# Optimization experiments

Measured on AMD Instinct MI355X. Metric: run time of the kernel, lower is better.

## Reference

```python
import jax, jax.numpy as jnp
import numpy as np
from jax import lax

B, T, V, E, H, DA, R, S, A, NR = 256, 64, 30000, 300, 512, 350, 16, 64, 16, 3


def setup_inputs() -> dict:
    key = jax.random.key(0)
    ks = jax.random.split(key, 24)

    def gn(k, shape, scale):
        return (jax.random.normal(k, shape) * scale).astype(jnp.float32)

    def xavier(k, shape):
        fan = sum(shape[-2:]) if len(shape) >= 2 else shape[0] * 2
        return (jax.random.uniform(k, shape, minval=-1.0, maxval=1.0)
                * np.sqrt(6.0 / fan)).astype(jnp.float32)

    s = 1.0 / np.sqrt(H)
    inp = {
        "tokens": jax.random.randint(ks[0], (B, T), 0, V),
        "lengths": jnp.full((B,), T, dtype=jnp.int32),
        "embedding": gn(ks[1], (V, E), 0.02),
        # BiLSTM layer 0 (input E), layer 1 (input 2H); gates order i,f,g,o (PyTorch)
        "Wih_l0f": gn(ks[2], (4 * H, E), s), "Whh_l0f": gn(ks[3], (4 * H, H), s), "b_l0f": jnp.zeros((4 * H,), jnp.float32),
        "Wih_l0b": gn(ks[4], (4 * H, E), s), "Whh_l0b": gn(ks[5], (4 * H, H), s), "b_l0b": jnp.zeros((4 * H,), jnp.float32),
        "Wih_l1f": gn(ks[6], (4 * H, 2 * H), s), "Whh_l1f": gn(ks[7], (4 * H, H), s), "b_l1f": jnp.zeros((4 * H,), jnp.float32),
        "Wih_l1b": gn(ks[8], (4 * H, 2 * H), s), "Whh_l1b": gn(ks[9], (4 * H, H), s), "b_l1b": jnp.zeros((4 * H,), jnp.float32),
        "ws1": xavier(ks[10], (DA, 2 * H)),
        "ws2": xavier(ks[11], (R, DA)),
        "caps_W": xavier(ks[12], (R, 2 * H, S * A)),
    }
    return inp


def _lstm_dir(x, Wih, Whh, b, reverse=False):
    # x: [T, B, D] -> hidden states [T, B, H]
    if reverse:
        x = x[::-1]
    h0 = jnp.zeros((x.shape[1], Whh.shape[1]), x.dtype)
    c0 = jnp.zeros_like(h0)

    def step(carry, xt):
        h, c = carry
        z = xt @ Wih.T + h @ Whh.T + b
        i, f, g, o = jnp.split(z, 4, axis=-1)
        c = jax.nn.sigmoid(f) * c + jax.nn.sigmoid(i) * jnp.tanh(g)
        h = jax.nn.sigmoid(o) * jnp.tanh(c)
        return (h, c), h

    _, hs = lax.scan(step, (h0, c0), x)
    return hs[::-1] if reverse else hs


def reference(tokens, lengths, embedding,
              Wih_l0f, Whh_l0f, b_l0f, Wih_l0b, Whh_l0b, b_l0b,
              Wih_l1f, Whh_l1f, b_l1f, Wih_l1b, Whh_l1b, b_l1b,
              ws1, ws2, caps_W):
    # Embedding + 2-layer BiLSTM (all lengths == T, so packing is a no-op).
    x = embedding[tokens].transpose(1, 0, 2)          # [T, B, E]
    l0 = jnp.concatenate([_lstm_dir(x, Wih_l0f, Whh_l0f, b_l0f),
                          _lstm_dir(x, Wih_l0b, Whh_l0b, b_l0b, True)], -1)
    l1 = jnp.concatenate([_lstm_dir(l0, Wih_l1f, Whh_l1f, b_l1f),
                          _lstm_dir(l0, Wih_l1b, Whh_l1b, b_l1b, True)], -1)
    outp = l1.transpose(1, 0, 2)                      # [B, T, 2H]

    # Self-attention pooling (note: original applies NO softmax on alphas).
    hbar = jnp.tanh(jnp.einsum('bte,ae->bta', outp, ws1))   # [B, T, DA]
    alphas = jnp.einsum('bta,ra->btr', hbar, ws2)           # [B, T, R]
    attention = alphas.transpose(0, 2, 1)                   # [B, R, T]
    sent = jnp.einsum('brt,bte->bre', attention, outp)      # [B, R, 2H]

    # Capsule votes + dynamic routing.
    votes = jnp.einsum('bri,rio->bro', sent, caps_W).reshape(B, R, S, A)
    logits = jnp.zeros((B, R, S), votes.dtype)
    for _ in range(NR):
        route = jax.nn.softmax(logits, axis=2)
        preact = jnp.einsum('brs,brsa->bsa', route, votes)  # [B, S, A]
        norm = jnp.linalg.norm(preact, axis=2, keepdims=True)
        act = preact / norm * (norm * norm / (0.5 + norm * norm))
        logits = logits + jnp.einsum('brsa,bsa->brs', votes, act)
    class_logits = jnp.linalg.norm(act, axis=-1)            # [B, S]
    return (sent, class_logits)
```

## Files before the change

kernel.cpp:

```cpp
#include <hip/hip_runtime.h>
#include <stdint.h>

#define PB 256
#define PT 64
#define PE 300
#define PH 512
#define PDA 350
#define PR 16
#define PS 64
#define PA 16

typedef __attribute__((ext_vector_type(8))) short short8;
typedef __attribute__((ext_vector_type(4))) float f4;
typedef unsigned long long u64;

__device__ __forceinline__ float bf2f(unsigned short u) {
    unsigned v = ((unsigned)u) << 16;
    return __builtin_bit_cast(float, v);
}
__device__ __forceinline__ unsigned short f2bf(float f) {
    unsigned u = __builtin_bit_cast(unsigned int, f);
    u = u + 0x7fffu + ((u >> 16) & 1u);
    return (unsigned short)(u >> 16);
}
__device__ __forceinline__ float sigf(float x) { return 1.f / (1.f + __expf(-x)); }
__device__ __forceinline__ float tanhf_(float x) { return 1.f - 2.f / (1.f + __expf(2.f * x)); }


__global__ __launch_bounds__(256) void k_embed(const int* __restrict__ tokens,
                                               const float* __restrict__ emb,
                                               unsigned short* __restrict__ X) {
    int idx = blockIdx.x * 256 + threadIdx.x;
    if (idx >= 16384 * 320) return;
    int row = idx / 320, e = idx - row * 320;
    int t = row >> 8, b = row & 255;
    float v = 0.f;
    if (e < 300) v = emb[(long)tokens[b * 64 + t] * 300 + e];
    X[idx] = f2bf(v);
}

__global__ __launch_bounds__(256) void k_cvt_pad(const float* __restrict__ src,
                                                 unsigned short* __restrict__ dst,
                                                 int N, int K, int N2, int K2) {
    int idx = blockIdx.x * 256 + threadIdx.x;
    if (idx >= N2 * K2) return;
    int n = idx / K2, k = idx - n * K2;
    float v = (n < N && k < K) ? src[(long)n * K + k] : 0.f;
    dst[idx] = f2bf(v);
}

__global__ __launch_bounds__(256) void k_capsT(const float* __restrict__ src,
                                               unsigned short* __restrict__ dst) {
    __shared__ float tile[32][33];
    int r = blockIdx.x, kb = blockIdx.y * 32, nb = blockIdx.z * 32;
    int tx = threadIdx.x & 31, ty = threadIdx.x >> 5;
    for (int i = 0; i < 32; i += 8)
        tile[ty + i][tx] = src[((long)r << 20) + (long)(kb + ty + i) * 1024 + nb + tx];
    __syncthreads();
    for (int i = 0; i < 32; i += 8)
        dst[((long)r << 20) + (long)(nb + ty + i) * 1024 + kb + tx] = f2bf(tile[tx][ty + i]);
}

__global__ __launch_bounds__(256) void k_whh_shuf(const float* __restrict__ W,
                                                  unsigned short* __restrict__ dst) {
    int idx = blockIdx.x * 256 + threadIdx.x;
    int el = idx & 7, lane = (idx >> 3) & 63, ks = (idx >> 9) & 15, nt = (idx >> 13) & 7, hs = idx >> 16;
    int gcol = (nt >> 1) * 512 + hs * 32 + (nt & 1) * 16 + (lane & 15);
    int k = ks * 32 + (lane >> 4) * 8 + el;
    dst[idx] = f2bf(W[(long)gcol * 512 + k]);
}

template <int OUT_BF16, int TANH>
__global__ __launch_bounds__(256) void k_gemm(const unsigned short* __restrict__ A,
                                              const unsigned short* __restrict__ W,
                                              void* __restrict__ Cv,
                                              const float* __restrict__ bias,
                                              int K, int lda, int ldc,
                                              long aOffZ, long wOffZ, long cOffZ, long bOffZ) {
    A += blockIdx.z * aOffZ;
    W += blockIdx.z * wOffZ;
    if (bias) bias += blockIdx.z * bOffZ;
    const long cbase = blockIdx.z * cOffZ;
    const int m0 = blockIdx.x * 128, n0 = blockIdx.y * 128;
    __shared__ unsigned short As[4096], Bs[4096];
    const int w = threadIdx.x >> 6, l = threadIdx.x & 63;
    const int wm = w & 1, wn = w >> 1;
    const int fr = l & 15, fk = (l >> 4) * 8;
    f4 acc[4][4] = {};
    for (int k0 = 0; k0 < K; k0 += 32) {
        __syncthreads();
#pragma unroll
        for (int i = 0; i < 2; i++) {
            int tI = w + i * 4;
            const unsigned short* ga = A + (long)(m0 + tI * 16 + fr) * lda + k0 + fk;
            const unsigned short* gb = W + (long)(n0 + tI * 16 + fr) * K + k0 + fk;
            *(short8*)&As[tI * 512 + l * 8] = *(const short8*)ga;
            *(short8*)&Bs[tI * 512 + l * 8] = *(const short8*)gb;
        }
        __syncthreads();
        short8 av[4], bv[4];
#pragma unroll
        for (int mt = 0; mt < 4; mt++) av[mt] = *(short8*)&As[(wm * 4 + mt) * 512 + l * 8];
#pragma unroll
        for (int nt = 0; nt < 4; nt++) bv[nt] = *(short8*)&Bs[(wn * 4 + nt) * 512 + l * 8];
#pragma unroll
        for (int mt = 0; mt < 4; mt++)
#pragma unroll
            for (int nt = 0; nt < 4; nt++)
                acc[mt][nt] = __builtin_amdgcn_mfma_f32_16x16x32_bf16(av[mt], bv[nt], acc[mt][nt], 0, 0, 0);
    }
#pragma unroll
    for (int mt = 0; mt < 4; mt++) {
        int row = m0 + wm * 64 + mt * 16 + (l >> 4) * 4;
#pragma unroll
        for (int nt = 0; nt < 4; nt++) {
            int col = n0 + wn * 64 + nt * 16 + (l & 15);
            float bb = bias ? bias[col] : 0.f;
#pragma unroll
            for (int i = 0; i < 4; i++) {
                float v = acc[mt][nt][i] + bb;
                if (TANH) v = tanhf_(v);
                long off = cbase + (long)(row + i) * ldc + col;
                if (OUT_BF16)
                    ((unsigned short*)Cv)[off] = f2bf(v);
                else
                    ((float*)Cv)[off] = v;
            }
        }
    }
}

__global__ __launch_bounds__(256, 1) void k_lstm(const unsigned short* __restrict__ Zx,
                                                 const unsigned short* __restrict__ Wshuf,
                                                 unsigned short* __restrict__ hsteps,
                                                 unsigned short* __restrict__ Lout,
                                                 unsigned* __restrict__ cnt) {
    extern __shared__ char smem[];
    unsigned short* Wl = (unsigned short*)smem;
    const int bid = blockIdx.x;
    const int dir = bid >> 6, bg = (bid >> 4) & 3, hs = bid & 15;
    const int tid = threadIdx.x;
    const int l = tid & 63;
    const int w = tid >> 6;
    const int mt2 = w & 1, hc2 = w >> 1;

    {
        const short8* src = (const short8*)(Wshuf + ((long)(dir * 16 + hs) << 16));
        short8* dst = (short8*)Wl;
        for (int i = tid; i < 8192; i += 256) dst[i] = src[i];
    }
    {
        unsigned short* hz = hsteps + (long)dir * (256 * 512);
        for (int i = tid; i < 1024; i += 256) {
            int r = i >> 4, c2 = i & 15;
            __hip_atomic_store((unsigned*)&hz[(bg * 64 + r) * 512 + hs * 32 + c2 * 2], 0u,
                               __ATOMIC_RELAXED, __HIP_MEMORY_SCOPE_AGENT);
        }
    }
    unsigned* myc = cnt + (dir * 4 + bg) * 32;
    asm volatile("s_waitcnt vmcnt(0)" ::: "memory");
    __syncthreads();
    if (tid == 0) __hip_atomic_fetch_add(myc, 1u, __ATOMIC_RELAXED, __HIP_MEMORY_SCOPE_AGENT);

    float c_reg[8];
#pragma unroll
    for (int i = 0; i < 8; i++) c_reg[i] = 0.f;

    const int jg = hs * 32 + hc2 * 16 + (l & 15);
    int rowg_[2][4];
#pragma unroll
    for (int i2 = 0; i2 < 2; i2++)
#pragma unroll
        for (int i = 0; i < 4; i++)
            rowg_[i2][i] = bg * 64 + (mt2 * 2 + i2) * 16 + (l >> 4) * 4 + i;

    for (int step = 0; step < 64; step++) {
        const int t_eff = dir ? (63 - step) : step;
        const unsigned short* zbase = Zx + ((long)dir * 16384 + (long)t_eff * 256) * 2048;

        unsigned short zpre[2][4][4];
#pragma unroll
        for (int i2 = 0; i2 < 2; i2++)
#pragma unroll
            for (int i = 0; i < 4; i++) {
                const unsigned short* zrow = zbase + (long)rowg_[i2][i] * 2048 + jg;
#pragma unroll
                for (int g = 0; g < 4; g++) zpre[i2][i][g] = zrow[g * 512];
            }

        if (tid == 0) {
            unsigned target = 16u * (unsigned)(step + 1);
            while (__hip_atomic_load(myc, __ATOMIC_RELAXED, __HIP_MEMORY_SCOPE_AGENT) < target) {}
        }
        __syncthreads();

        const unsigned short* hb = hsteps + ((long)step * 2 + dir) * (256 * 512);
        const unsigned short* pa0 = hb + (bg * 64 + (mt2 * 2 + 0) * 16 + (l & 15)) * 512 + (l >> 4) * 8;
        const unsigned short* pa1 = hb + (bg * 64 + (mt2 * 2 + 1) * 16 + (l & 15)) * 512 + (l >> 4) * 8;
        short8 a0[16], a1[16];
#pragma unroll
        for (int ks = 0; ks < 16; ks++) {
            a0[ks] = *(const short8*)(pa0 + ks * 32);
            a1[ks] = *(const short8*)(pa1 + ks * 32);
        }
        asm volatile("" ::: "memory");

        f4 acc[2][4] = {};
#pragma unroll
        for (int ks = 0; ks < 16; ks++) {
#pragma unroll
            for (int s = 0; s < 4; s++) {
                int nt = s * 2 + hc2;
                short8 b = *(short8*)&Wl[((nt * 16 + ks) * 64 + l) * 8];
                acc[0][s] = __builtin_amdgcn_mfma_f32_16x16x32_bf16(a0[ks], b, acc[0][s], 0, 0, 0);
                acc[1][s] = __builtin_amdgcn_mfma_f32_16x16x32_bf16(a1[ks], b, acc[1][s], 0, 0, 0);
            }
        }

        unsigned short hv[2][4];
        unsigned short* hw = hsteps + ((long)(step + 1) * 2 + dir) * (256 * 512);
#pragma unroll
        for (int i2 = 0; i2 < 2; i2++)
#pragma unroll
            for (int i = 0; i < 4; i++) {
                float zi = acc[i2][0][i] + bf2f(zpre[i2][i][0]);
                float zf = acc[i2][1][i] + bf2f(zpre[i2][i][1]);
                float zg = acc[i2][2][i] + bf2f(zpre[i2][i][2]);
                float zo = acc[i2][3][i] + bf2f(zpre[i2][i][3]);
                int ci = i2 * 4 + i;
                float c = sigf(zf) * c_reg[ci] + sigf(zi) * tanhf_(zg);
                c_reg[ci] = c;
                float h = sigf(zo) * tanhf_(c);
                unsigned short hb16 = f2bf(h);
                hv[i2][i] = hb16;
                __hip_atomic_store(&hw[(long)rowg_[i2][i] * 512 + jg], hb16,
                                   __ATOMIC_RELAXED, __HIP_MEMORY_SCOPE_AGENT);
            }
        asm volatile("s_waitcnt vmcnt(0)" ::: "memory");
        __syncthreads();
        if (tid == 0) __hip_atomic_fetch_add(myc, 1u, __ATOMIC_RELAXED, __HIP_MEMORY_SCOPE_AGENT);

#pragma unroll
        for (int i2 = 0; i2 < 2; i2++)
#pragma unroll
            for (int i = 0; i < 4; i++)
                Lout[((long)t_eff * 256 + rowg_[i2][i]) * 1024 + dir * 512 + jg] = hv[i2][i];
    }
}

__global__ __launch_bounds__(256) void k_alphas(const unsigned short* __restrict__ hbar,
                                                const unsigned short* __restrict__ ws2,
                                                float* __restrict__ att) {
    int w = threadIdx.x >> 6, l = threadIdx.x & 63;
    int mtile = blockIdx.x * 4 + w;
    f4 acc = {};
    const unsigned short* arow = hbar + (long)(mtile * 16 + (l & 15)) * 384 + (l >> 4) * 8;
    const unsigned short* brow = ws2 + (long)(l & 15) * 384 + (l >> 4) * 8;
    for (int ks = 0; ks < 12; ks++) {
        short8 a = *(const short8*)&arow[ks * 32];
        short8 b = *(const short8*)&brow[ks * 32];
        acc = __builtin_amdgcn_mfma_f32_16x16x32_bf16(a, b, acc, 0, 0, 0);
    }
    int r = l & 15;
#pragma unroll
    for (int i = 0; i < 4; i++) {
        int bt = mtile * 16 + (l >> 4) * 4 + i;
        int b = bt & 255, t = bt >> 8;
        att[((long)b * 16 + r) * 64 + t] = acc[i];
    }
}

__global__ __launch_bounds__(256) void k_sent(const float* __restrict__ att,
                                              const unsigned short* __restrict__ L1,
                                              float* __restrict__ sent,
                                              unsigned short* __restrict__ sentb) {
    int b = blockIdx.x, n0 = blockIdx.y * 128;
    __shared__ float al[1024];
    for (int i = threadIdx.x; i < 1024; i += 256) al[i] = att[(long)b * 1024 + i];
    __syncthreads();
    int n = n0 + (threadIdx.x & 127);
    int rh = (threadIdx.x >> 7) * 8;
    float acc[8] = {};
    for (int t = 0; t < 64; t++) {
        float x = bf2f(L1[((long)t * 256 + b) * 1024 + n]);
#pragma unroll
        for (int r = 0; r < 8; r++) acc[r] += al[(rh + r) * 64 + t] * x;
    }
#pragma unroll
    for (int r = 0; r < 8; r++) {
        long o = ((long)b * 16 + rh + r) * 1024 + n;
        sent[o] = acc[r];
        sentb[o] = f2bf(acc[r]);
    }
}

__global__ __launch_bounds__(256) void k_route(const float* __restrict__ votes,
                                               float* __restrict__ clog) {
    __shared__ float v[16384];
    __shared__ float logits[1024];
    __shared__ float route[1024];
    __shared__ float pre[1024];
    __shared__ float act[1024];
    __shared__ float cl[64];
    int b = blockIdx.x, tid = threadIdx.x;
    for (int i = tid; i < 4096; i += 256) ((f4*)v)[i] = ((const f4*)(votes + (long)b * 16384))[i];
    for (int i = tid; i < 1024; i += 256) logits[i] = 0.f;
    __syncthreads();
    for (int it = 0; it < 3; it++) {
        if (tid < 16) {
            float m = -1e30f;
            for (int s = 0; s < 64; s++) m = fmaxf(m, logits[tid * 64 + s]);
            float sum = 0.f;
            for (int s = 0; s < 64; s++) {
                float e = __expf(logits[tid * 64 + s] - m);
                route[tid * 64 + s] = e;
                sum += e;
            }
            float inv = 1.f / sum;
            for (int s = 0; s < 64; s++) route[tid * 64 + s] *= inv;
        }
        __syncthreads();
#pragma unroll
        for (int k = 0; k < 4; k++) {
            int p = k * 256 + tid;
            int s = p >> 4, a = p & 15;
            float acc = 0.f;
            for (int r = 0; r < 16; r++) acc += route[r * 64 + s] * v[(r * 64 + s) * 16 + a];
            pre[p] = acc;
        }
        __syncthreads();
        if (tid < 64) {
            float nsq = 0.f;
            for (int a = 0; a < 16; a++) nsq += pre[tid * 16 + a] * pre[tid * 16 + a];
            float norm = sqrtf(nsq);
            float sc = norm / (0.5f + nsq);
            for (int a = 0; a < 16; a++) act[tid * 16 + a] = pre[tid * 16 + a] * sc;
            cl[tid] = nsq / (0.5f + nsq);
        }
        __syncthreads();
#pragma unroll
        for (int k = 0; k < 4; k++) {
            int p = k * 256 + tid;
            int r = p >> 6, s = p & 63;
            float acc = 0.f;
            for (int a = 0; a < 16; a++) acc += v[(r * 64 + s) * 16 + a] * act[s * 16 + a];
            logits[p] += acc;
        }
        __syncthreads();
    }
    if (tid < 64) clog[(long)b * 64 + tid] = cl[tid];
}

extern "C" void kernel_launch(void* const* d_in, const int* in_sizes, int n_in,
                              void* d_out, int out_size, void* d_ws, size_t ws_size,
                              hipStream_t stream) {
    const int* tokens = (const int*)d_in[0];
    const float* embedding = (const float*)d_in[2];
    const float* Wih_l0f = (const float*)d_in[3];
    const float* Whh_l0f = (const float*)d_in[4];
    const float* b_l0f = (const float*)d_in[5];
    const float* Wih_l0b = (const float*)d_in[6];
    const float* Whh_l0b = (const float*)d_in[7];
    const float* b_l0b = (const float*)d_in[8];
    const float* Wih_l1f = (const float*)d_in[9];
    const float* Whh_l1f = (const float*)d_in[10];
    const float* b_l1f = (const float*)d_in[11];
    const float* Wih_l1b = (const float*)d_in[12];
    const float* Whh_l1b = (const float*)d_in[13];
    const float* b_l1b = (const float*)d_in[14];
    const float* ws1 = (const float*)d_in[15];
    const float* ws2 = (const float*)d_in[16];
    const float* caps_W = (const float*)d_in[17];
    float* out = (float*)d_out;

    char* ws = (char*)d_ws;
    size_t o = 0;
    unsigned short* Xb16 = (unsigned short*)(ws + o); o += (size_t)16384 * 320 * 2;
    unsigned short* ZxL = (unsigned short*)(ws + o); size_t zx_off = o; o += (size_t)2 * 16384 * 2048 * 2;
    unsigned short* L0 = (unsigned short*)(ws + o); o += (size_t)16384 * 1024 * 2;
    unsigned short* L1 = (unsigned short*)(ws + o); o += (size_t)16384 * 1024 * 2;
    unsigned short* Wl0b = (unsigned short*)(ws + o); o += (size_t)2 * 2048 * 320 * 2;
    unsigned short* Wl1b = (unsigned short*)(ws + o); o += (size_t)2 * 2048 * 1024 * 2;
    unsigned short* Wsh0 = (unsigned short*)(ws + o); o += (size_t)2 * 1048576 * 2;
    unsigned short* Wsh1 = (unsigned short*)(ws + o); o += (size_t)2 * 1048576 * 2;
    unsigned short* ws1b = (unsigned short*)(ws + o); o += (size_t)384 * 1024 * 2;
    unsigned short* ws2b = (unsigned short*)(ws + o); o += (size_t)16 * 384 * 2 + 192;
    float* biasc = (float*)(ws + o); o += (size_t)4 * 2048 * 4;
    unsigned* cnts = (unsigned*)(ws + o); o += 4096;
    unsigned short* hsteps = (unsigned short*)(ws + o);
    unsigned short* capsT = (unsigned short*)(ws + o);
    o += (size_t)65 * 2 * 256 * 512 * 2;
    unsigned short* hbarb = (unsigned short*)(ws + zx_off);
    float* att = (float*)(ws + zx_off + (size_t)16384 * 384 * 2);
    unsigned short* sentb = (unsigned short*)(ws + zx_off + (size_t)16384 * 384 * 2 + 1048576);
    float* votes = (float*)(ws + zx_off + (size_t)16384 * 384 * 2 + 1048576 + (size_t)256 * 16 * 1024 * 2);

    hipMemsetAsync(cnts, 0, 4096, stream);

    k_embed<<<16384 * 320 / 256, 256, 0, stream>>>(tokens, embedding, Xb16);
    k_cvt_pad<<<(2048 * 320 + 255) / 256, 256, 0, stream>>>(Wih_l0f, Wl0b, 2048, 300, 2048, 320);
    k_cvt_pad<<<(2048 * 320 + 255) / 256, 256, 0, stream>>>(Wih_l0b, Wl0b + (size_t)2048 * 320, 2048, 300, 2048, 320);
    k_cvt_pad<<<(2048 * 1024 + 255) / 256, 256, 0, stream>>>(Wih_l1f, Wl1b, 2048, 1024, 2048, 1024);
    k_cvt_pad<<<(2048 * 1024 + 255) / 256, 256, 0, stream>>>(Wih_l1b, Wl1b + (size_t)2048 * 1024, 2048, 1024, 2048, 1024);
    k_cvt_pad<<<(384 * 1024 + 255) / 256, 256, 0, stream>>>(ws1, ws1b, 350, 1024, 384, 1024);
    k_cvt_pad<<<(16 * 384 + 255) / 256, 256, 0, stream>>>(ws2, ws2b, 16, 350, 16, 384);
    k_whh_shuf<<<4096, 256, 0, stream>>>(Whh_l0f, Wsh0);
    k_whh_shuf<<<4096, 256, 0, stream>>>(Whh_l0b, Wsh0 + 1048576);
    k_whh_shuf<<<4096, 256, 0, stream>>>(Whh_l1f, Wsh1);
    k_whh_shuf<<<4096, 256, 0, stream>>>(Whh_l1b, Wsh1 + 1048576);
    hipMemcpyAsync(biasc + 0, b_l0f, 2048 * 4, hipMemcpyDeviceToDevice, stream);
    hipMemcpyAsync(biasc + 2048, b_l0b, 2048 * 4, hipMemcpyDeviceToDevice, stream);
    hipMemcpyAsync(biasc + 4096, b_l1f, 2048 * 4, hipMemcpyDeviceToDevice, stream);
    hipMemcpyAsync(biasc + 6144, b_l1b, 2048 * 4, hipMemcpyDeviceToDevice, stream);

    hipFuncSetAttribute(reinterpret_cast<const void*>(k_lstm),
                        hipFuncAttributeMaxDynamicSharedMemorySize, 131072);

    k_gemm<1, 0><<<dim3(128, 16, 2), 256, 0, stream>>>(
        Xb16, Wl0b, ZxL, biasc, 320, 320, 2048,
        0L, (long)2048 * 320, (long)16384 * 2048, 2048L);
    k_lstm<<<128, 256, 131072, stream>>>(ZxL, Wsh0, hsteps, L0, cnts);
    k_gemm<1, 0><<<dim3(128, 16, 2), 256, 0, stream>>>(
        L0, Wl1b, ZxL, biasc + 4096, 1024, 1024, 2048,
        0L, (long)2048 * 1024, (long)16384 * 2048, 2048L);
    k_lstm<<<128, 256, 131072, stream>>>(ZxL, Wsh1, hsteps, L1, cnts + 256);
    k_capsT<<<dim3(16, 32, 32), 256, 0, stream>>>(caps_W, capsT);
    k_gemm<1, 1><<<dim3(128, 3, 1), 256, 0, stream>>>(
        L1, ws1b, hbarb, nullptr, 1024, 1024, 384, 0L, 0L, 0L, 0L);
    k_alphas<<<256, 256, 0, stream>>>(hbarb, ws2b, att);
    k_sent<<<dim3(256, 8), 256, 0, stream>>>(att, L1, out, sentb);
    k_gemm<0, 0><<<dim3(2, 8, 16), 256, 0, stream>>>(
        sentb, capsT, votes, nullptr, 1024, 16384, 16384,
        1024L, 1048576L, 1024L, 0L);
    k_route<<<256, 256, 0, stream>>>(votes, out + (size_t)4194304);
}
```

Measured before the change: 1.785 ms.

## Replace LSTM atomic counter barrier with per-block flags and staged coalesced h stores

The persistent LSTM kernel's inter-block barrier changes from a shared atomic counter incremented by 16 blocks to per-block step flags, each on its own cache line. A whole wavefront polls all 16 flags in parallel with a wave vote, which removes contention from the atomic adds. New h values are staged through an LDS tile so each thread writes 8-byte coalesced stores to the global h buffer and to the layer output, replacing scattered 2-byte atomic stores. The cost is an extra LDS round trip and block barrier per step, plus slightly more shared memory.

```diff
diff --git a/kernel.cpp b/kernel.cpp
--- a/kernel.cpp
+++ b/kernel.cpp
@@ -134,11 +134,13 @@
                                                  const unsigned short* __restrict__ Wshuf,
                                                  unsigned short* __restrict__ hsteps,
                                                  unsigned short* __restrict__ Lout,
-                                                 unsigned* __restrict__ cnt) {
+                                                 unsigned* __restrict__ flags) {
     extern __shared__ char smem[];
     unsigned short* Wl = (unsigned short*)smem;
+    unsigned short* hrep = (unsigned short*)(smem + 131072);
     const int bid = blockIdx.x;
     const int dir = bid >> 6, bg = (bid >> 4) & 3, hs = bid & 15;
+    const int grp = dir * 4 + bg;
     const int tid = threadIdx.x;
     const int l = tid & 63;
     const int w = tid >> 6;
@@ -157,10 +159,11 @@
                                __ATOMIC_RELAXED, __HIP_MEMORY_SCOPE_AGENT);
         }
     }
-    unsigned* myc = cnt + (dir * 4 + bg) * 32;
+    unsigned* myflag = flags + (grp * 16 + hs) * 16;
+    unsigned* pollp = flags + (grp * 16 + (l & 15)) * 16;
     asm volatile("s_waitcnt vmcnt(0)" ::: "memory");
     __syncthreads();
-    if (tid == 0) __hip_atomic_fetch_add(myc, 1u, __ATOMIC_RELAXED, __HIP_MEMORY_SCOPE_AGENT);
+    if (tid == 0) __hip_atomic_store(myflag, 1u, __ATOMIC_RELAXED, __HIP_MEMORY_SCOPE_AGENT);
 
     float c_reg[8];
 #pragma unroll
@@ -173,6 +176,9 @@
 #pragma unroll
         for (int i = 0; i < 4; i++)
             rowg_[i2][i] = bg * 64 + (mt2 * 2 + i2) * 16 + (l >> 4) * 4 + i;
+
+    const int sr0 = tid >> 3, sr1 = 32 + (tid >> 3);
+    const int so = (tid & 7) * 4;
 
     for (int step = 0; step < 64; step++) {
         const int t_eff = dir ? (63 - step) : step;
@@ -188,9 +194,12 @@
                 for (int g = 0; g < 4; g++) zpre[i2][i][g] = zrow[g * 512];
             }
 
-        if (tid == 0) {
-            unsigned target = 16u * (unsigned)(step + 1);
-            while (__hip_atomic_load(myc, __ATOMIC_RELAXED, __HIP_MEMORY_SCOPE_AGENT) < target) {}
+        if (w == 0) {
+            const unsigned target = (unsigned)(step + 1);
+            while (true) {
+                unsigned f = __hip_atomic_load(pollp, __ATOMIC_RELAXED, __HIP_MEMORY_SCOPE_AGENT);
+                if (__all((int)(f >= target))) break;
+            }
         }
         __syncthreads();
 
@@ -217,8 +226,6 @@
             }
         }
 
-        unsigned short hv[2][4];
-        unsigned short* hw = hsteps + ((long)(step + 1) * 2 + dir) * (256 * 512);
 #pragma unroll
         for (int i2 = 0; i2 < 2; i2++)
 #pragma unroll
@@ -231,20 +238,26 @@
                 float c = sigf(zf) * c_reg[ci] + sigf(zi) * tanhf_(zg);
                 c_reg[ci] = c;
                 float h = sigf(zo) * tanhf_(c);
-                unsigned short hb16 = f2bf(h);
-                hv[i2][i] = hb16;
-                __hip_atomic_store(&hw[(long)rowg_[i2][i] * 512 + jg], hb16,
-                                   __ATOMIC_RELAXED, __HIP_MEMORY_SCOPE_AGENT);
-            }
+                int lr = (mt2 * 2 + i2) * 16 + (l >> 4) * 4 + i;
+                int lc = hc2 * 16 + (l & 15);
+                hrep[lr * 36 + lc] = f2bf(h);
+            }
+        __syncthreads();
+
+        u64 v0 = *(const u64*)&hrep[sr0 * 36 + so];
+        u64 v1 = *(const u64*)&hrep[sr1 * 36 + so];
+        unsigned short* hw = hsteps + ((long)(step + 1) * 2 + dir) * (256 * 512);
+        __hip_atomic_store((u64*)&hw[(bg * 64 + sr0) * 512 + hs * 32 + so], v0,
+                           __ATOMIC_RELAXED, __HIP_MEMORY_SCOPE_AGENT);
+        __hip_atomic_store((u64*)&hw[(bg * 64 + sr1) * 512 + hs * 32 + so], v1,
+                           __ATOMIC_RELAXED, __HIP_MEMORY_SCOPE_AGENT);
         asm volatile("s_waitcnt vmcnt(0)" ::: "memory");
         __syncthreads();
-        if (tid == 0) __hip_atomic_fetch_add(myc, 1u, __ATOMIC_RELAXED, __HIP_MEMORY_SCOPE_AGENT);
-
-#pragma unroll
-        for (int i2 = 0; i2 < 2; i2++)
-#pragma unroll
-            for (int i = 0; i < 4; i++)
-                Lout[((long)t_eff * 256 + rowg_[i2][i]) * 1024 + dir * 512 + jg] = hv[i2][i];
+        if (tid == 0)
+            __hip_atomic_store(myflag, (unsigned)(step + 2), __ATOMIC_RELAXED, __HIP_MEMORY_SCOPE_AGENT);
+
+        *(u64*)&Lout[((long)t_eff * 256 + bg * 64 + sr0) * 1024 + dir * 512 + hs * 32 + so] = v0;
+        *(u64*)&Lout[((long)t_eff * 256 + bg * 64 + sr1) * 1024 + dir * 512 + hs * 32 + so] = v1;
     }
 }
 
@@ -386,7 +399,7 @@
     unsigned short* ws1b = (unsigned short*)(ws + o); o += (size_t)384 * 1024 * 2;
     unsigned short* ws2b = (unsigned short*)(ws + o); o += (size_t)16 * 384 * 2 + 192;
     float* biasc = (float*)(ws + o); o += (size_t)4 * 2048 * 4;
-    unsigned* cnts = (unsigned*)(ws + o); o += 4096;
+    unsigned* flags = (unsigned*)(ws + o); o += 16384;
     unsigned short* hsteps = (unsigned short*)(ws + o);
     unsigned short* capsT = (unsigned short*)(ws + o);
     o += (size_t)65 * 2 * 256 * 512 * 2;
@@ -395,7 +408,7 @@
     unsigned short* sentb = (unsigned short*)(ws + zx_off + (size_t)16384 * 384 * 2 + 1048576);
     float* votes = (float*)(ws + zx_off + (size_t)16384 * 384 * 2 + 1048576 + (size_t)256 * 16 * 1024 * 2);
 
-    hipMemsetAsync(cnts, 0, 4096, stream);
+    hipMemsetAsync(flags, 0, 16384, stream);
 
     k_embed<<<16384 * 320 / 256, 256, 0, stream>>>(tokens, embedding, Xb16);
     k_cvt_pad<<<(2048 * 320 + 255) / 256, 256, 0, stream>>>(Wih_l0f, Wl0b, 2048, 300, 2048, 320);
@@ -414,16 +427,16 @@
     hipMemcpyAsync(biasc + 6144, b_l1b, 2048 * 4, hipMemcpyDeviceToDevice, stream);
 
     hipFuncSetAttribute(reinterpret_cast<const void*>(k_lstm),
-                        hipFuncAttributeMaxDynamicSharedMemorySize, 131072);
+                        hipFuncAttributeMaxDynamicSharedMemorySize, 135680);
 
     k_gemm<1, 0><<<dim3(128, 16, 2), 256, 0, stream>>>(
         Xb16, Wl0b, ZxL, biasc, 320, 320, 2048,
         0L, (long)2048 * 320, (long)16384 * 2048, 2048L);
-    k_lstm<<<128, 256, 131072, stream>>>(ZxL, Wsh0, hsteps, L0, cnts);
+    k_lstm<<<128, 256, 135680, stream>>>(ZxL, Wsh0, hsteps, L0, flags);
     k_gemm<1, 0><<<dim3(128, 16, 2), 256, 0, stream>>>(
         L0, Wl1b, ZxL, biasc + 4096, 1024, 1024, 2048,
         0L, (long)2048 * 1024, (long)16384 * 2048, 2048L);
-    k_lstm<<<128, 256, 131072, stream>>>(ZxL, Wsh1, hsteps, L1, cnts + 256);
+    k_lstm<<<128, 256, 135680, stream>>>(ZxL, Wsh1, hsteps, L1, flags + 2048);
     k_capsT<<<dim3(16, 32, 32), 256, 0, stream>>>(caps_W, capsT);
     k_gemm<1, 1><<<dim3(128, 3, 1), 256, 0, stream>>>(
         L1, ws1b, hbarb, nullptr, 1024, 1024, 384, 0L, 0L, 0L, 0L);
```

After: 1.773 ms. No clear change (-0.6%).
